# Optimization experiments

Hardware: AMD Instinct MI355X
Metric: run time of the kernel (lower is better)

Reference implementation:

```python
import jax, jax.numpy as jnp
import numpy as np

N_RES = 3      # n_resblock (weights SHARED across layers, matching [block]*n in torch)
N_E = 1024     # n_embeddings
E_DIM = 64     # dim_embeddings
P = 4
BETA = 0.25
B = 16384      # batch rows
IN = 128       # input_size
DENC = 512     # dim_encoder
DOUT = E_DIM * P  # dim_encoder_out = 256


def setup_inputs() -> dict:
    key = jax.random.key(0)
    ks = jax.random.split(key, 16)
    def w(k, o, i):
        return jax.random.normal(k, (o, i), jnp.float32) * 0.02
    return {
        "x": jax.random.normal(ks[0], (B, IN), jnp.float32),
        "a": jax.random.normal(ks[1], (B, IN), jnp.float32),
        "scale": 1.0 + 0.1 * jax.random.normal(ks[2], (IN,), jnp.float32),
        "shift": 0.01 * jax.random.normal(ks[3], (IN,), jnp.float32),
        "enc_win_w": w(ks[4], DENC, IN), "enc_win_b": jnp.zeros((DENC,), jnp.float32),
        "enc_ain_w": w(ks[5], DENC, IN), "enc_ain_b": jnp.zeros((DENC,), jnp.float32),
        "enc_wres_w": w(ks[6], DENC, DENC), "enc_wres_b": jnp.zeros((DENC,), jnp.float32),
        "enc_wres_g": jnp.ones((DENC,), jnp.float32), "enc_wres_be": jnp.zeros((DENC,), jnp.float32),
        "enc_ares_w": w(ks[7], DENC, DENC), "enc_ares_b": jnp.zeros((DENC,), jnp.float32),
        "enc_ares_g": jnp.ones((DENC,), jnp.float32), "enc_ares_be": jnp.zeros((DENC,), jnp.float32),
        "enc_out_w": w(ks[8], DOUT, DENC), "enc_out_b": jnp.zeros((DOUT,), jnp.float32),
        "dec1_w": w(ks[9], DENC, DOUT), "dec1_b": jnp.zeros((DENC,), jnp.float32),
        "dec_res_w": w(ks[10], DENC, DENC), "dec_res_b": jnp.zeros((DENC,), jnp.float32),
        "dec_res_g": jnp.ones((DENC,), jnp.float32), "dec_res_be": jnp.zeros((DENC,), jnp.float32),
        "dec2_w": w(ks[11], IN, DENC), "dec2_b": jnp.zeros((IN,), jnp.float32),
        "codebook": jax.random.uniform(ks[12], (N_E, E_DIM), jnp.float32, -1.0 / N_E, 1.0 / N_E),
    }


def _ln(h, g, b, eps=1e-5):
    m = jnp.mean(h, axis=-1, keepdims=True)
    v = jnp.var(h, axis=-1, keepdims=True)
    return (h - m) * jax.lax.rsqrt(v + eps) * g + b


def _resblock(x, w, b, g, be):
    # Linear -> LayerNorm -> ReLU, residual add
    h = x @ w.T + b
    return x + jax.nn.relu(_ln(h, g, be))


def reference(x, a, scale, shift,
              enc_win_w, enc_win_b, enc_ain_w, enc_ain_b,
              enc_wres_w, enc_wres_b, enc_wres_g, enc_wres_be,
              enc_ares_w, enc_ares_b, enc_ares_g, enc_ares_be,
              enc_out_w, enc_out_b,
              dec1_w, dec1_b,
              dec_res_w, dec_res_b, dec_res_g, dec_res_be,
              dec2_w, dec2_b, codebook):
    sg = jax.lax.stop_gradient
    # --- input normalization ---
    xs = (x - shift) / scale
    # --- Encoder (weight path modulated by activation-magnitude path) ---
    av = a @ enc_ain_w.T + enc_ain_b
    h = xs @ enc_win_w.T + enc_win_b
    for _ in range(N_RES):  # shared weights per stack, interleaved mul
        av = _resblock(av, enc_ares_w, enc_ares_b, enc_ares_g, enc_ares_be)
        h = _resblock(h, enc_wres_w, enc_wres_b, enc_wres_g, enc_wres_be) * av
    z_e = h @ enc_out_w.T + enc_out_b  # (B, P*E_DIM)
    # --- Vector quantization (cdist + argmin + gather) ---
    zf = z_e.reshape(-1, E_DIM)  # (B*P, E_DIM)
    d = (jnp.sum(zf * zf, axis=1, keepdims=True)
         + jnp.sum(codebook * codebook, axis=1)
         - 2.0 * zf @ codebook.T)  # (B*P, N_E)
    idx = jnp.argmin(d, axis=1)  # (B*P,)
    z_q = codebook[idx].reshape(z_e.shape)
    loss = (jnp.mean((sg(z_q) - z_e) ** 2)
            + BETA * jnp.mean((z_q - sg(z_e)) ** 2))
    z_q_st = z_e + sg(z_q - z_e)  # straight-through
    counts = jnp.zeros((N_E,), jnp.float32).at[idx].add(1.0)
    e_mean = counts / zf.shape[0]
    perplexity = jnp.exp(-jnp.sum(e_mean * jnp.log(e_mean + 1e-10)))
    # --- Decoder ---
    hd = z_q_st @ dec1_w.T + dec1_b
    for _ in range(N_RES):
        hd = _resblock(hd, dec_res_w, dec_res_b, dec_res_g, dec_res_be)
    x_hat = hd @ dec2_w.T + dec2_b
    x_hat = scale * x_hat + shift
    return (loss, x_hat, perplexity, z_q_st, idx)
```

## Files before the change

kernel.cpp:

```cpp
#include <hip/hip_runtime.h>
#include <hip/hip_bf16.h>
#include <math.h>

static constexpr int BROWS = 16384;
static constexpr int IND   = 128;
static constexpr int DE    = 512;
static constexpr int DOUTD = 256;
static constexpr int ED    = 64;
static constexpr int NE    = 1024;

static constexpr size_t O_XHAT = 1;
static constexpr size_t O_PERP = 2097153;
static constexpr size_t O_ZQ   = 2097154;
static constexpr size_t O_IDX  = 6291458;

typedef __attribute__((ext_vector_type(8))) short short8v;
typedef __attribute__((ext_vector_type(4))) float f32x4;
typedef __attribute__((ext_vector_type(4))) unsigned short ushort4v;
typedef __attribute__((ext_vector_type(8))) unsigned short ushort8v;

__device__ inline float wave_sum(float v) {
#pragma unroll
    for (int o = 32; o >= 1; o >>= 1) v += __shfl_xor(v, o, 64);
    return v;
}

__device__ inline unsigned short f2bf(float f) {
    unsigned u = __float_as_uint(f);
    return (unsigned short)((u + 0x7FFFu + ((u >> 16) & 1u)) >> 16);
}
__device__ inline float bf2f(unsigned short b) {
    return __uint_as_float(((unsigned)b) << 16);
}
struct Split3 { unsigned short b0, b1, b2; };
__device__ inline Split3 split3(float v) {
    Split3 s;
    s.b0 = f2bf(v);  float r  = v - bf2f(s.b0);
    s.b1 = f2bf(r);  float r2 = r - bf2f(s.b1);
    s.b2 = f2bf(r2);
    return s;
}

template<int K, int EPI>
__device__ inline void gemm8_body(const unsigned short* __restrict__ A0, const unsigned short* __restrict__ A1,
                                  const unsigned short* __restrict__ A2,
                                  const unsigned short* __restrict__ W0, const unsigned short* __restrict__ W1,
                                  const unsigned short* __restrict__ W2,
                                  const float* __restrict__ bias, float* __restrict__ Cf,
                                  unsigned short* __restrict__ S0, unsigned short* __restrict__ S1,
                                  unsigned short* __restrict__ S2, int N,
                                  short (*As)[128 * 40], short (*Ws)[128 * 40])
{
    const int t = threadIdx.x;
    const int bm = blockIdx.x << 7, bn = blockIdx.y << 7;
    const int lane = t & 63, wid = t >> 6;
    const int wm = (wid >> 1) << 6, wn = (wid & 1) << 6;
    const int lr = lane & 15, lg = lane >> 4;
    const unsigned short* Ap[3] = {A0, A1, A2};
    const unsigned short* Wp[3] = {W0, W1, W2};
    f32x4 acc[4][4] = {};
    for (int k0 = 0; k0 < K; k0 += 32) {
#pragma unroll
        for (int p = 0; p < 3; ++p) {
#pragma unroll
            for (int s = 0; s < 2; ++s) {
                int c = t + (s << 8);
                int row = c >> 2, kc = (c & 3) << 3;
                *(short8v*)&As[p][row * 40 + kc] =
                    *(const short8v*)(Ap[p] + (size_t)(bm + row) * K + k0 + kc);
                *(short8v*)&Ws[p][row * 40 + kc] =
                    *(const short8v*)(Wp[p] + (size_t)(bn + row) * K + k0 + kc);
            }
        }
        __syncthreads();
        short8v bfr[3][4];
#pragma unroll
        for (int p = 0; p < 3; ++p)
#pragma unroll
            for (int nj = 0; nj < 4; ++nj)
                bfr[p][nj] = *(const short8v*)&Ws[p][(wn + nj * 16 + lr) * 40 + lg * 8];
#pragma unroll
        for (int mi = 0; mi < 4; ++mi) {
            short8v a0 = *(const short8v*)&As[0][(wm + mi * 16 + lr) * 40 + lg * 8];
            short8v a1 = *(const short8v*)&As[1][(wm + mi * 16 + lr) * 40 + lg * 8];
            short8v a2 = *(const short8v*)&As[2][(wm + mi * 16 + lr) * 40 + lg * 8];
#pragma unroll
            for (int nj = 0; nj < 4; ++nj) {
                f32x4 c = acc[mi][nj];
                c = __builtin_amdgcn_mfma_f32_16x16x32_bf16(a2, bfr[1][nj], c, 0, 0, 0);
                c = __builtin_amdgcn_mfma_f32_16x16x32_bf16(a1, bfr[2][nj], c, 0, 0, 0);
                c = __builtin_amdgcn_mfma_f32_16x16x32_bf16(a1, bfr[1][nj], c, 0, 0, 0);
                c = __builtin_amdgcn_mfma_f32_16x16x32_bf16(a2, bfr[0][nj], c, 0, 0, 0);
                c = __builtin_amdgcn_mfma_f32_16x16x32_bf16(a0, bfr[2][nj], c, 0, 0, 0);
                c = __builtin_amdgcn_mfma_f32_16x16x32_bf16(a1, bfr[0][nj], c, 0, 0, 0);
                c = __builtin_amdgcn_mfma_f32_16x16x32_bf16(a0, bfr[1][nj], c, 0, 0, 0);
                c = __builtin_amdgcn_mfma_f32_16x16x32_bf16(a0, bfr[0][nj], c, 0, 0, 0);
                acc[mi][nj] = c;
            }
        }
        __syncthreads();
    }
#pragma unroll
    for (int mi = 0; mi < 4; ++mi)
#pragma unroll
        for (int nj = 0; nj < 4; ++nj)
#pragma unroll
            for (int r = 0; r < 4; ++r) {
                int m = bm + wm + mi * 16 + lg * 4 + r;
                int n = bn + wn + nj * 16 + lr;
                float v = acc[mi][nj][r] + bias[n];
                if (EPI == 0) {
                    Cf[(size_t)m * N + n] = v;
                } else {
                    Split3 sp = split3(v);
                    S0[(size_t)m * N + n] = sp.b0;
                    S1[(size_t)m * N + n] = sp.b1;
                    S2[(size_t)m * N + n] = sp.b2;
                }
            }
}

template<int K>
__global__ __launch_bounds__(256)
void gemm8_k(const unsigned short* __restrict__ A0, const unsigned short* __restrict__ A1,
             const unsigned short* __restrict__ A2,
             const unsigned short* __restrict__ W0, const unsigned short* __restrict__ W1,
             const unsigned short* __restrict__ W2,
             const float* __restrict__ bias, float* __restrict__ C, int N)
{
    __shared__ short As[3][128 * 40];
    __shared__ short Ws[3][128 * 40];
    gemm8_body<K, 0>(A0, A1, A2, W0, W1, W2, bias, C, nullptr, nullptr, nullptr, N, As, Ws);
}

struct G8 { const unsigned short *A0, *A1, *A2, *W0, *W1, *W2; const float* bias;
            float* Cf; unsigned short *S0, *S1, *S2; };

template<int K, int EPI>
__global__ __launch_bounds__(256)
void gemm8pair_k(G8 ga, G8 gb, int N)
{
    __shared__ short As[3][128 * 40];
    __shared__ short Ws[3][128 * 40];
    const G8& g = (blockIdx.z == 0) ? ga : gb;
    gemm8_body<K, EPI>(g.A0, g.A1, g.A2, g.W0, g.W1, g.W2, g.bias, g.Cf,
                       g.S0, g.S1, g.S2, N, As, Ws);
}

template<int K, int EPI>
__global__ __launch_bounds__(256)
void gemmbf_k(const short* __restrict__ A, const short* __restrict__ W,
              const float* __restrict__ bias, float* __restrict__ C, int N,
              unsigned short* __restrict__ Cb,
              const float* __restrict__ escale, const float* __restrict__ eshift)
{
    __shared__ short As[128 * 40];
    __shared__ short Ws[128 * 40];
    const int t = threadIdx.x;
    const int bm = blockIdx.x << 7, bn = blockIdx.y << 7;
    const int lane = t & 63, wid = t >> 6;
    const int wm = (wid >> 1) << 6, wn = (wid & 1) << 6;
    const int lr = lane & 15, lg = lane >> 4;
    f32x4 acc[4][4] = {};
    for (int k0 = 0; k0 < K; k0 += 32) {
#pragma unroll
        for (int s = 0; s < 2; ++s) {
            int c = t + (s << 8);
            int row = c >> 2, kc = (c & 3) << 3;
            *(short8v*)&As[row * 40 + kc] = *(const short8v*)(A + (size_t)(bm + row) * K + k0 + kc);
            *(short8v*)&Ws[row * 40 + kc] = *(const short8v*)(W + (size_t)(bn + row) * K + k0 + kc);
        }
        __syncthreads();
        short8v af[4], bf[4];
#pragma unroll
        for (int mi = 0; mi < 4; ++mi) af[mi] = *(const short8v*)&As[(wm + mi * 16 + lr) * 40 + lg * 8];
#pragma unroll
        for (int nj = 0; nj < 4; ++nj) bf[nj] = *(const short8v*)&Ws[(wn + nj * 16 + lr) * 40 + lg * 8];
#pragma unroll
        for (int mi = 0; mi < 4; ++mi)
#pragma unroll
            for (int nj = 0; nj < 4; ++nj)
                acc[mi][nj] = __builtin_amdgcn_mfma_f32_16x16x32_bf16(af[mi], bf[nj], acc[mi][nj], 0, 0, 0);
        __syncthreads();
    }
#pragma unroll
    for (int mi = 0; mi < 4; ++mi)
#pragma unroll
        for (int nj = 0; nj < 4; ++nj)
#pragma unroll
            for (int r = 0; r < 4; ++r) {
                int m = bm + wm + mi * 16 + lg * 4 + r;
                int n = bn + wn + nj * 16 + lr;
                float v = acc[mi][nj][r] + bias[n];
                if (EPI == 2) v = escale[n] * v + eshift[n];
                C[(size_t)m * N + n] = v;
                if (EPI == 1) Cb[(size_t)m * N + n] = f2bf(v);
            }
}

__global__ __launch_bounds__(256)
void prep2_k(const float* __restrict__ x, const float* __restrict__ scale,
             const float* __restrict__ shift,
             unsigned short* __restrict__ x0, unsigned short* __restrict__ x1,
             unsigned short* __restrict__ x2,
             const float* __restrict__ a,
             unsigned short* __restrict__ a0, unsigned short* __restrict__ a1,
             unsigned short* __restrict__ a2)
{
    if (blockIdx.x < 2048) {
        int g = blockIdx.x * 256 + threadIdx.x;
        float4 v = *(const float4*)(x + (size_t)g * 4);
        int col = (g * 4) & (IND - 1);
        float vals[4] = {v.x, v.y, v.z, v.w};
        ushort4v o0, o1, o2;
#pragma unroll
        for (int i = 0; i < 4; ++i) {
            float xs = (vals[i] - shift[col + i]) / scale[col + i];
            Split3 s = split3(xs);
            o0[i] = s.b0; o1[i] = s.b1; o2[i] = s.b2;
        }
        *(ushort4v*)(x0 + (size_t)g * 4) = o0;
        *(ushort4v*)(x1 + (size_t)g * 4) = o1;
        *(ushort4v*)(x2 + (size_t)g * 4) = o2;
    } else {
        int g = (blockIdx.x - 2048) * 256 + threadIdx.x;
        float4 v = *(const float4*)(a + (size_t)g * 4);
        float vals[4] = {v.x, v.y, v.z, v.w};
        ushort4v o0, o1, o2;
#pragma unroll
        for (int i = 0; i < 4; ++i) {
            Split3 s = split3(vals[i]);
            o0[i] = s.b0; o1[i] = s.b1; o2[i] = s.b2;
        }
        *(ushort4v*)(a0 + (size_t)g * 4) = o0;
        *(ushort4v*)(a1 + (size_t)g * 4) = o1;
        *(ushort4v*)(a2 + (size_t)g * 4) = o2;
    }
}

__global__ __launch_bounds__(256)
void wsplit_k(const float* __restrict__ ain_w, const float* __restrict__ win_w,
              const float* __restrict__ ares_w, const float* __restrict__ wres_w,
              const float* __restrict__ out_w,
              unsigned short* __restrict__ wsb)
{
    int g4 = blockIdx.x * 256 + threadIdx.x;
    const float* src; unsigned short *d0, *d1, *d2; int base;
    if (g4 < 16384)       { src = ain_w;  d0 = wsb;           d1 = wsb + 65536;   d2 = wsb + 131072;  base = 0; }
    else if (g4 < 32768)  { src = win_w;  d0 = wsb + 196608;  d1 = wsb + 262144;  d2 = wsb + 327680;  base = 16384; }
    else if (g4 < 98304)  { src = ares_w; d0 = wsb + 393216;  d1 = wsb + 655360;  d2 = wsb + 917504;  base = 32768; }
    else if (g4 < 163840) { src = wres_w; d0 = wsb + 1179648; d1 = wsb + 1441792; d2 = wsb + 1703936; base = 98304; }
    else                  { src = out_w;  d0 = wsb + 1966080; d1 = wsb + 2097152; d2 = wsb + 2228224; base = 163840; }
    int l4 = g4 - base;
    float4 v = *(const float4*)(src + (size_t)l4 * 4);
    float vals[4] = {v.x, v.y, v.z, v.w};
    ushort4v o0, o1, o2;
#pragma unroll
    for (int i = 0; i < 4; ++i) {
        Split3 s = split3(vals[i]);
        o0[i] = s.b0; o1[i] = s.b1; o2[i] = s.b2;
    }
    *(ushort4v*)(d0 + (size_t)l4 * 4) = o0;
    *(ushort4v*)(d1 + (size_t)l4 * 4) = o1;
    *(ushort4v*)(d2 + (size_t)l4 * 4) = o2;
}

__global__ __launch_bounds__(256)
void cvt3_k(const float* __restrict__ dec1_w, const float* __restrict__ dres_w,
            const float* __restrict__ dec2_w,
            unsigned short* __restrict__ w1b, unsigned short* __restrict__ wrb,
            unsigned short* __restrict__ w2b)
{
    int g = blockIdx.x * 256 + threadIdx.x;
    if (g < 131072)       w1b[g] = f2bf(dec1_w[g]);
    else if (g < 393216)  wrb[g - 131072] = f2bf(dres_w[g - 131072]);
    else if (g < 458752)  w2b[g - 393216] = f2bf(dec2_w[g - 393216]);
}

__global__ __launch_bounds__(256)
void ln_enc2s_k(const float* __restrict__ T1, const float* __restrict__ T2,
                unsigned short* __restrict__ a0, unsigned short* __restrict__ a1,
                unsigned short* __restrict__ a2,
                unsigned short* __restrict__ h0, unsigned short* __restrict__ h1,
                unsigned short* __restrict__ h2,
                const float* __restrict__ ag, const float* __restrict__ abe,
                const float* __restrict__ wg, const float* __restrict__ wbe)
{
    const int lane = threadIdx.x & 63;
    const int row  = (blockIdx.x << 2) + (threadIdx.x >> 6);
    const int col  = lane << 3;
    const size_t base = (size_t)row * DE + col;
    float t[8];
    { float4 p0 = *(const float4*)(T1 + base); float4 p1 = *(const float4*)(T1 + base + 4);
      t[0]=p0.x; t[1]=p0.y; t[2]=p0.z; t[3]=p0.w; t[4]=p1.x; t[5]=p1.y; t[6]=p1.z; t[7]=p1.w; }
    float s = 0.f;
#pragma unroll
    for (int i = 0; i < 8; ++i) s += t[i];
    s = wave_sum(s);
    float mean = s * (1.0f / 512.0f);
    float vs = 0.f;
#pragma unroll
    for (int i = 0; i < 8; ++i) { float d = t[i] - mean; vs += d * d; }
    vs = wave_sum(vs);
    float rstd = 1.0f / sqrtf(vs * (1.0f / 512.0f) + 1e-5f);
    float avn[8];
    {
        ushort8v b0 = *(const ushort8v*)(a0 + base);
        ushort8v b1 = *(const ushort8v*)(a1 + base);
        ushort8v b2 = *(const ushort8v*)(a2 + base);
        ushort8v o0, o1, o2;
#pragma unroll
        for (int i = 0; i < 8; ++i) {
            float avv = bf2f(b0[i]) + bf2f(b1[i]) + bf2f(b2[i]);
            float lnv = (t[i] - mean) * rstd * ag[col + i] + abe[col + i];
            avn[i] = avv + fmaxf(lnv, 0.0f);
            Split3 sp = split3(avn[i]);
            o0[i] = sp.b0; o1[i] = sp.b1; o2[i] = sp.b2;
        }
        *(ushort8v*)(a0 + base) = o0;
        *(ushort8v*)(a1 + base) = o1;
        *(ushort8v*)(a2 + base) = o2;
    }
    { float4 p0 = *(const float4*)(T2 + base); float4 p1 = *(const float4*)(T2 + base + 4);
      t[0]=p0.x; t[1]=p0.y; t[2]=p0.z; t[3]=p0.w; t[4]=p1.x; t[5]=p1.y; t[6]=p1.z; t[7]=p1.w; }
    s = 0.f;
#pragma unroll
    for (int i = 0; i < 8; ++i) s += t[i];
    s = wave_sum(s);
    float mean2 = s * (1.0f / 512.0f);
    vs = 0.f;
#pragma unroll
    for (int i = 0; i < 8; ++i) { float d = t[i] - mean2; vs += d * d; }
    vs = wave_sum(vs);
    float rstd2 = 1.0f / sqrtf(vs * (1.0f / 512.0f) + 1e-5f);
    {
        ushort8v b0 = *(const ushort8v*)(h0 + base);
        ushort8v b1 = *(const ushort8v*)(h1 + base);
        ushort8v b2 = *(const ushort8v*)(h2 + base);
        ushort8v o0, o1, o2;
#pragma unroll
        for (int i = 0; i < 8; ++i) {
            float hv  = bf2f(b0[i]) + bf2f(b1[i]) + bf2f(b2[i]);
            float lnv = (t[i] - mean2) * rstd2 * wg[col + i] + wbe[col + i];
            float hn  = (hv + fmaxf(lnv, 0.0f)) * avn[i];
            Split3 sp = split3(hn);
            o0[i] = sp.b0; o1[i] = sp.b1; o2[i] = sp.b2;
        }
        *(ushort8v*)(h0 + base) = o0;
        *(ushort8v*)(h1 + base) = o1;
        *(ushort8v*)(h2 + base) = o2;
    }
}

__global__ __launch_bounds__(256)
void ln_dec_k(const float* __restrict__ t_, float* __restrict__ h,
              const float* __restrict__ g, const float* __restrict__ be,
              unsigned short* __restrict__ hb)
{
    const int lane = threadIdx.x & 63;
    const int row  = (blockIdx.x << 2) + (threadIdx.x >> 6);
    const int col  = lane << 3;
    const size_t base = (size_t)row * DE + col;
    float t[8];
    { float4 p0 = *(const float4*)(t_ + base); float4 p1 = *(const float4*)(t_ + base + 4);
      t[0]=p0.x; t[1]=p0.y; t[2]=p0.z; t[3]=p0.w; t[4]=p1.x; t[5]=p1.y; t[6]=p1.z; t[7]=p1.w; }
    float s = 0.f;
#pragma unroll
    for (int i = 0; i < 8; ++i) s += t[i];
    s = wave_sum(s);
    float mean = s * (1.0f / 512.0f);
    float vs = 0.f;
#pragma unroll
    for (int i = 0; i < 8; ++i) { float d = t[i] - mean; vs += d * d; }
    vs = wave_sum(vs);
    float rstd = 1.0f / sqrtf(vs * (1.0f / 512.0f) + 1e-5f);
    float4 p0 = *(const float4*)(h + base); float4 p1 = *(const float4*)(h + base + 4);
    float hv[8] = {p0.x,p0.y,p0.z,p0.w,p1.x,p1.y,p1.z,p1.w};
    float hn[8];
    ushort8v ob;
#pragma unroll
    for (int i = 0; i < 8; ++i) {
        float lnv = (t[i] - mean) * rstd * g[col + i] + be[col + i];
        hn[i] = hv[i] + fmaxf(lnv, 0.0f);
        ob[i] = f2bf(hn[i]);
    }
    float4 o0 = {hn[0],hn[1],hn[2],hn[3]}, o1 = {hn[4],hn[5],hn[6],hn[7]};
    *(float4*)(h + base) = o0; *(float4*)(h + base + 4) = o1;
    *(ushort8v*)(hb + base) = ob;
}

__global__ __launch_bounds__(256)
void c2z_k(const float* __restrict__ cb, float* __restrict__ c2, int* __restrict__ counts,
           unsigned short* __restrict__ cbS0, unsigned short* __restrict__ cbS1,
           unsigned short* __restrict__ cbS2)
{
    int j = blockIdx.x * 256 + threadIdx.x;
    if (j < NE) {
        float s = 0.f;
        const float* p = cb + (size_t)j * ED;
#pragma unroll
        for (int d = 0; d < ED; ++d) s = fmaf(p[d], p[d], s);
        c2[j] = s;
        counts[j] = 0;
#pragma unroll
        for (int dc = 0; dc < 64; dc += 4) {
            float4 v = *(const float4*)(p + dc);
            float vals[4] = {v.x, v.y, v.z, v.w};
            ushort4v o0, o1, o2;
#pragma unroll
            for (int i = 0; i < 4; ++i) {
                Split3 sp = split3(vals[i]);
                o0[i] = sp.b0; o1[i] = sp.b1; o2[i] = sp.b2;
            }
            *(ushort4v*)(cbS0 + (size_t)j * 64 + dc) = o0;
            *(ushort4v*)(cbS1 + (size_t)j * 64 + dc) = o1;
            *(ushort4v*)(cbS2 + (size_t)j * 64 + dc) = o2;
        }
    }
}

__global__ __launch_bounds__(256)
void vq_k(const float* __restrict__ ze, const float* __restrict__ cb, const float* __restrict__ c2,
          const unsigned short* __restrict__ cbS0, const unsigned short* __restrict__ cbS1,
          const unsigned short* __restrict__ cbS2,
          float* __restrict__ idx_dst, float* __restrict__ zst_dst,
          unsigned short* __restrict__ zb,
          int* __restrict__ counts, float* __restrict__ partials)
{
    __shared__ unsigned short zA[3][64 * 64];
    __shared__ unsigned short cB[3][64 * 64];
    __shared__ float z2s[64];
    __shared__ float c2s[64];
    __shared__ int   bidxs[64];
    __shared__ float red[4];
    const int t = threadIdx.x;
    const int lane = t & 63, w = t >> 6;
    const size_t row0 = (size_t)blockIdx.x * 64;

#pragma unroll
    for (int s = 0; s < 2; ++s) {
        int c = t + (s << 8);
        int row = c >> 3, kb = c & 7;
        float4 v0 = *(const float4*)(ze + (row0 + row) * 64 + kb * 8);
        float4 v1 = *(const float4*)(ze + (row0 + row) * 64 + kb * 8 + 4);
        float vals[8] = {v0.x, v0.y, v0.z, v0.w, v1.x, v1.y, v1.z, v1.w};
        ushort8v o0, o1, o2;
#pragma unroll
        for (int i = 0; i < 8; ++i) {
            Split3 sp = split3(vals[i]);
            o0[i] = sp.b0; o1[i] = sp.b1; o2[i] = sp.b2;
        }
        int base = row * 64 + ((kb ^ (row & 7)) << 3);
        *(ushort8v*)&zA[0][base] = o0;
        *(ushort8v*)&zA[1][base] = o1;
        *(ushort8v*)&zA[2][base] = o2;
    }
    if (t < 64) {
        float z2 = 0.f;
        const float* zp = ze + (row0 + t) * 64;
#pragma unroll 8
        for (int d = 0; d < 64; ++d) z2 = fmaf(zp[d], zp[d], z2);
        z2s[t] = z2;
    }
    __syncthreads();

    short8v af[2][3];
    {
        int row = (w << 4) + (lane & 15);
#pragma unroll
        for (int ks = 0; ks < 2; ++ks) {
            int kb = (lane >> 4) + ks * 4;
            int base = row * 64 + ((kb ^ (row & 7)) << 3);
#pragma unroll
            for (int p = 0; p < 3; ++p)
                af[ks][p] = *(const short8v*)&zA[p][base];
        }
    }

    float best[4] = {INFINITY, INFINITY, INFINITY, INFINITY};
    int   bid[4]  = {0, 0, 0, 0};
    for (int t0 = 0; t0 < NE; t0 += 64) {
        __syncthreads();
#pragma unroll
        for (int s = 0; s < 2; ++s) {
            int c = t + (s << 8);
            int code = c >> 3, kb = c & 7;
            int gbase = (t0 + code) * 64 + kb * 8;
            int lbase = code * 64 + ((kb ^ (code & 7)) << 3);
            *(ushort8v*)&cB[0][lbase] = *(const ushort8v*)(cbS0 + gbase);
            *(ushort8v*)&cB[1][lbase] = *(const ushort8v*)(cbS1 + gbase);
            *(ushort8v*)&cB[2][lbase] = *(const ushort8v*)(cbS2 + gbase);
        }
        if (t < 64) c2s[t] = c2[t0 + t];
        __syncthreads();

#pragma unroll
        for (int ct = 0; ct < 4; ++ct) {
            f32x4 acc = {0.f, 0.f, 0.f, 0.f};
            int code = (ct << 4) + (lane & 15);
#pragma unroll
            for (int ks = 0; ks < 2; ++ks) {
                int kb = (lane >> 4) + ks * 4;
                int base = code * 64 + ((kb ^ (code & 7)) << 3);
                short8v b0 = *(const short8v*)&cB[0][base];
                short8v b1 = *(const short8v*)&cB[1][base];
                short8v b2 = *(const short8v*)&cB[2][base];
                acc = __builtin_amdgcn_mfma_f32_16x16x32_bf16(af[ks][2], b1, acc, 0, 0, 0);
                acc = __builtin_amdgcn_mfma_f32_16x16x32_bf16(af[ks][1], b2, acc, 0, 0, 0);
                acc = __builtin_amdgcn_mfma_f32_16x16x32_bf16(af[ks][1], b1, acc, 0, 0, 0);
                acc = __builtin_amdgcn_mfma_f32_16x16x32_bf16(af[ks][2], b0, acc, 0, 0, 0);
                acc = __builtin_amdgcn_mfma_f32_16x16x32_bf16(af[ks][0], b2, acc, 0, 0, 0);
                acc = __builtin_amdgcn_mfma_f32_16x16x32_bf16(af[ks][1], b0, acc, 0, 0, 0);
                acc = __builtin_amdgcn_mfma_f32_16x16x32_bf16(af[ks][0], b1, acc, 0, 0, 0);
                acc = __builtin_amdgcn_mfma_f32_16x16x32_bf16(af[ks][0], b0, acc, 0, 0, 0);
            }
            float c2v = c2s[(ct << 4) + (lane & 15)];
            int gcode = t0 + (ct << 4) + (lane & 15);
#pragma unroll
            for (int r = 0; r < 4; ++r) {
                float z2v = z2s[(w << 4) + ((lane >> 4) << 2) + r];
                float term = __fadd_rn(z2v, c2v);
                float dist = __fsub_rn(term, __fmul_rn(2.0f, acc[r]));
                if (dist < best[r]) { best[r] = dist; bid[r] = gcode; }
            }
        }
    }
#pragma unroll
    for (int r = 0; r < 4; ++r) {
        float bd = best[r]; int bi = bid[r];
#pragma unroll
        for (int m = 1; m < 16; m <<= 1) {
            float od = __shfl_xor(bd, m, 64);
            int   oi = __shfl_xor(bi, m, 64);
            if (od < bd || (od == bd && oi < bi)) { bd = od; bi = oi; }
        }
        if ((lane & 15) == 0) {
            int row = (w << 4) + ((lane >> 4) << 2) + r;
            bidxs[row] = bi;
            idx_dst[row0 + row] = (float)bi;
            atomicAdd(&counts[bi], 1);
        }
    }
    __syncthreads();
    const int row = t >> 2, cq = t & 3;
    const int bi = bidxs[row];
    float lsum = 0.f;
#pragma unroll
    for (int dd = 0; dd < 16; dd += 4) {
        int d0 = (cq << 4) + dd;
        float4 q4 = *(const float4*)(cb + (size_t)bi * 64 + d0);
        float qv[4] = {q4.x, q4.y, q4.z, q4.w};
        float4 zv4 = *(const float4*)(ze + (row0 + row) * 64 + d0);
        float zvv[4] = {zv4.x, zv4.y, zv4.z, zv4.w};
        float zst[4];
#pragma unroll
        for (int i = 0; i < 4; ++i) {
            float zv = zvv[i];
            float df = qv[i] - zv;
            lsum = fmaf(df, df, lsum);
            zst[i] = __fadd_rn(zv, __fsub_rn(qv[i], zv));
            zb[(row0 + row) * 64 + d0 + i] = f2bf(zst[i]);
        }
        float2 o0 = {zst[0], zst[1]}, o1 = {zst[2], zst[3]};
        *(float2*)(zst_dst + (row0 + row) * 64 + d0) = o0;
        *(float2*)(zst_dst + (row0 + row) * 64 + d0 + 2) = o1;
    }
    lsum = wave_sum(lsum);
    if ((t & 63) == 0) red[t >> 6] = lsum;
    __syncthreads();
    if (t == 0) partials[blockIdx.x] = ((red[0] + red[1]) + red[2]) + red[3];
}

__global__ __launch_bounds__(256)
void fin_k(const float* __restrict__ partials, const int* __restrict__ counts,
           float* __restrict__ loss_out, float* __restrict__ perp_out)
{
    __shared__ float red[4];
    __shared__ float red2[4];
    const int tid = threadIdx.x;
    float v = 0.f;
    for (int c = tid; c < 1024; c += 256) v += partials[c];
    float s = wave_sum(v);
    if ((tid & 63) == 0) red[tid >> 6] = s;
    float ep = 0.f;
    for (int c = tid; c < NE; c += 256) {
        float e = (float)counts[c] * (1.0f / 65536.0f);
        ep += e * logf(e + 1e-10f);
    }
    ep = wave_sum(ep);
    if ((tid & 63) == 0) red2[tid >> 6] = ep;
    __syncthreads();
    if (tid == 0) {
        float S = ((red[0] + red[1]) + red[2]) + red[3];
        float E = ((red2[0] + red2[1]) + red2[2]) + red2[3];
        loss_out[0] = 1.25f * (S * (1.0f / 4194304.0f));
        perp_out[0] = expf(-E);
    }
}

extern "C" void kernel_launch(void* const* d_in, const int* in_sizes, int n_in,
                              void* d_out, int out_size, void* d_ws, size_t ws_size,
                              hipStream_t stream)
{
    const float* x       = (const float*)d_in[0];
    const float* a       = (const float*)d_in[1];
    const float* scale   = (const float*)d_in[2];
    const float* shift   = (const float*)d_in[3];
    const float* win_w   = (const float*)d_in[4];
    const float* win_b   = (const float*)d_in[5];
    const float* ain_w   = (const float*)d_in[6];
    const float* ain_b   = (const float*)d_in[7];
    const float* wres_w  = (const float*)d_in[8];
    const float* wres_b  = (const float*)d_in[9];
    const float* wres_g  = (const float*)d_in[10];
    const float* wres_be = (const float*)d_in[11];
    const float* ares_w  = (const float*)d_in[12];
    const float* ares_b  = (const float*)d_in[13];
    const float* ares_g  = (const float*)d_in[14];
    const float* ares_be = (const float*)d_in[15];
    const float* out_w   = (const float*)d_in[16];
    const float* out_b   = (const float*)d_in[17];
    const float* dec1_w  = (const float*)d_in[18];
    const float* dec1_b  = (const float*)d_in[19];
    const float* dres_w  = (const float*)d_in[20];
    const float* dres_b  = (const float*)d_in[21];
    const float* dres_g  = (const float*)d_in[22];
    const float* dres_be = (const float*)d_in[23];
    const float* dec2_w  = (const float*)d_in[24];
    const float* dec2_b  = (const float*)d_in[25];
    const float* cb      = (const float*)d_in[26];

    float* ws = (float*)d_ws;
    unsigned short* u = (unsigned short*)d_ws;
    unsigned short* avS0 = u;
    unsigned short* avS1 = u + 8388608;
    unsigned short* avS2 = u + 16777216;
    unsigned short* hS0  = u + 25165824;
    unsigned short* hS1  = u + 33554432;
    unsigned short* hS2  = u + 41943040;
    float* T1 = ws + 25165824;
    float* T2 = ws + 29360128;
    float* ZE = ws + 25165824;
    unsigned short* aS0  = u + 50331648, *aS1  = u + 52428800, *aS2  = u + 54525952;
    unsigned short* xsS0 = u + 56623104, *xsS1 = u + 58720256, *xsS2 = u + 60817408;
    unsigned short* ZB  = u;
    unsigned short* w1b = u + 4194304;
    unsigned short* wrb = u + 4325376;
    unsigned short* w2b = u + 4587520;
    float* t_dec = ws + 4194304;
    float* hd    = ws + 12582912;
    unsigned short* Hb = (unsigned short*)(ws + 29360128);
    unsigned short* wsb = u + 67108864;
    unsigned short* ainS0 = wsb,            *ainS1 = wsb + 65536,  *ainS2 = wsb + 131072;
    unsigned short* winS0 = wsb + 196608,   *winS1 = wsb + 262144, *winS2 = wsb + 327680;
    unsigned short* areS0 = wsb + 393216,   *areS1 = wsb + 655360, *areS2 = wsb + 917504;
    unsigned short* wreS0 = wsb + 1179648,  *wreS1 = wsb + 1441792,*wreS2 = wsb + 1703936;
    unsigned short* outS0 = wsb + 1966080,  *outS1 = wsb + 2097152,*outS2 = wsb + 2228224;
    float* c2v      = ws + 34800000;
    int*   counts   = (int*)(ws + 34801024);
    float* partials = ws + 34802048;
    unsigned short* cbS0 = u + 69606144;
    unsigned short* cbS1 = u + 69671680;
    unsigned short* cbS2 = u + 69737216;

    float* dout = (float*)d_out;

    wsplit_k<<<768, 256, 0, stream>>>(ain_w, win_w, ares_w, wres_w, out_w, wsb);
    prep2_k<<<4096, 256, 0, stream>>>(x, scale, shift, xsS0, xsS1, xsS2, a, aS0, aS1, aS2);
    {
        G8 ga = {aS0, aS1, aS2, ainS0, ainS1, ainS2, ain_b, nullptr, avS0, avS1, avS2};
        G8 gb = {xsS0, xsS1, xsS2, winS0, winS1, winS2, win_b, nullptr, hS0, hS1, hS2};
        gemm8pair_k<128, 1><<<dim3(128, 4, 2), 256, 0, stream>>>(ga, gb, DE);
    }
    for (int r = 0; r < 3; ++r) {
        for (int half = 0; half < 2; ++half) {
            const size_t mo = (size_t)half * 8192 * DE;
            G8 ga = {avS0 + mo, avS1 + mo, avS2 + mo, areS0, areS1, areS2, ares_b, T1, nullptr, nullptr, nullptr};
            G8 gb = {hS0 + mo,  hS1 + mo,  hS2 + mo,  wreS0, wreS1, wreS2, wres_b, T2, nullptr, nullptr, nullptr};
            gemm8pair_k<512, 0><<<dim3(64, 4, 2), 256, 0, stream>>>(ga, gb, DE);
            ln_enc2s_k<<<2048, 256, 0, stream>>>(T1, T2,
                avS0 + mo, avS1 + mo, avS2 + mo, hS0 + mo, hS1 + mo, hS2 + mo,
                ares_g, ares_be, wres_g, wres_be);
        }
    }
    gemm8_k<512><<<dim3(128, 2), 256, 0, stream>>>(hS0, hS1, hS2, outS0, outS1, outS2, out_b, ZE, DOUTD);
    c2z_k<<<4, 256, 0, stream>>>(cb, c2v, counts, cbS0, cbS1, cbS2);
    vq_k<<<1024, 256, 0, stream>>>(ZE, cb, c2v, cbS0, cbS1, cbS2,
                                   dout + O_IDX, dout + O_ZQ, ZB, counts, partials);
    fin_k<<<1, 256, 0, stream>>>(partials, counts, dout, dout + O_PERP);
    cvt3_k<<<1792, 256, 0, stream>>>(dec1_w, dres_w, dec2_w, w1b, wrb, w2b);
    gemmbf_k<256, 1><<<dim3(128, 4), 256, 0, stream>>>(
        (const short*)ZB, (const short*)w1b, dec1_b, hd, DE, Hb, nullptr, nullptr);
    for (int r = 0; r < 3; ++r) {
        gemmbf_k<512, 0><<<dim3(128, 4), 256, 0, stream>>>(
            (const short*)Hb, (const short*)wrb, dres_b, t_dec, DE, nullptr, nullptr, nullptr);
        ln_dec_k<<<4096, 256, 0, stream>>>(t_dec, hd, dres_g, dres_be, Hb);
    }
    gemmbf_k<512, 2><<<dim3(128, 1), 256, 0, stream>>>(
        (const short*)Hb, (const short*)w2b, dec2_b, dout + O_XHAT, IND, nullptr, scale, shift);
}
```

Measured before the change: 817.2 us.

## Merge prep kernels and double-buffer codebook tiles in VQ kernel

Folds the weight split, input split and codebook norm/split kernels into one launch, which removes two kernel launches and their gaps. In the VQ kernel, codebook tiles are now double-buffered in shared memory: the next tile is loaded into registers while MFMAs run on the current one, and only one barrier is taken per tile instead of two. The c2 values are read straight from global memory rather than staged in shared memory. The cvt3 launch is moved earlier in the stream; this does not change the total work.

Result: faster. 789.8 us (-3.4%).

```diff
diff --git a/kernel.cpp b/kernel.cpp
--- a/kernel.cpp
+++ b/kernel.cpp
@@ -199,32 +199,32 @@
 }
 
 __global__ __launch_bounds__(256)
-void prep2_k(const float* __restrict__ x, const float* __restrict__ scale,
-             const float* __restrict__ shift,
-             unsigned short* __restrict__ x0, unsigned short* __restrict__ x1,
-             unsigned short* __restrict__ x2,
-             const float* __restrict__ a,
-             unsigned short* __restrict__ a0, unsigned short* __restrict__ a1,
-             unsigned short* __restrict__ a2)
-{
-    if (blockIdx.x < 2048) {
-        int g = blockIdx.x * 256 + threadIdx.x;
-        float4 v = *(const float4*)(x + (size_t)g * 4);
-        int col = (g * 4) & (IND - 1);
-        float vals[4] = {v.x, v.y, v.z, v.w};
-        ushort4v o0, o1, o2;
-#pragma unroll
-        for (int i = 0; i < 4; ++i) {
-            float xs = (vals[i] - shift[col + i]) / scale[col + i];
-            Split3 s = split3(xs);
-            o0[i] = s.b0; o1[i] = s.b1; o2[i] = s.b2;
-        }
-        *(ushort4v*)(x0 + (size_t)g * 4) = o0;
-        *(ushort4v*)(x1 + (size_t)g * 4) = o1;
-        *(ushort4v*)(x2 + (size_t)g * 4) = o2;
-    } else {
-        int g = (blockIdx.x - 2048) * 256 + threadIdx.x;
-        float4 v = *(const float4*)(a + (size_t)g * 4);
+void pre_k(const float* __restrict__ x, const float* __restrict__ scale,
+           const float* __restrict__ shift,
+           unsigned short* __restrict__ x0, unsigned short* __restrict__ x1,
+           unsigned short* __restrict__ x2,
+           const float* __restrict__ a,
+           unsigned short* __restrict__ a0, unsigned short* __restrict__ a1,
+           unsigned short* __restrict__ a2,
+           const float* __restrict__ ain_w, const float* __restrict__ win_w,
+           const float* __restrict__ ares_w, const float* __restrict__ wres_w,
+           const float* __restrict__ out_w, unsigned short* __restrict__ wsb,
+           const float* __restrict__ cb, float* __restrict__ c2, int* __restrict__ counts,
+           unsigned short* __restrict__ cbS0, unsigned short* __restrict__ cbS1,
+           unsigned short* __restrict__ cbS2)
+{
+    const int b = blockIdx.x;
+    const int t = threadIdx.x;
+    if (b < 768) {
+        int g4 = b * 256 + t;
+        const float* src; unsigned short *d0, *d1, *d2; int base;
+        if (g4 < 16384)       { src = ain_w;  d0 = wsb;           d1 = wsb + 65536;   d2 = wsb + 131072;  base = 0; }
+        else if (g4 < 32768)  { src = win_w;  d0 = wsb + 196608;  d1 = wsb + 262144;  d2 = wsb + 327680;  base = 16384; }
+        else if (g4 < 98304)  { src = ares_w; d0 = wsb + 393216;  d1 = wsb + 655360;  d2 = wsb + 917504;  base = 32768; }
+        else if (g4 < 163840) { src = wres_w; d0 = wsb + 1179648; d1 = wsb + 1441792; d2 = wsb + 1703936; base = 98304; }
+        else                  { src = out_w;  d0 = wsb + 1966080; d1 = wsb + 2097152; d2 = wsb + 2228224; base = 163840; }
+        int l4 = g4 - base;
+        float4 v = *(const float4*)(src + (size_t)l4 * 4);
         float vals[4] = {v.x, v.y, v.z, v.w};
         ushort4v o0, o1, o2;
 #pragma unroll
@@ -232,37 +232,65 @@
             Split3 s = split3(vals[i]);
             o0[i] = s.b0; o1[i] = s.b1; o2[i] = s.b2;
         }
-        *(ushort4v*)(a0 + (size_t)g * 4) = o0;
-        *(ushort4v*)(a1 + (size_t)g * 4) = o1;
-        *(ushort4v*)(a2 + (size_t)g * 4) = o2;
-    }
-}
-
-__global__ __launch_bounds__(256)
-void wsplit_k(const float* __restrict__ ain_w, const float* __restrict__ win_w,
-              const float* __restrict__ ares_w, const float* __restrict__ wres_w,
-              const float* __restrict__ out_w,
-              unsigned short* __restrict__ wsb)
-{
-    int g4 = blockIdx.x * 256 + threadIdx.x;
-    const float* src; unsigned short *d0, *d1, *d2; int base;
-    if (g4 < 16384)       { src = ain_w;  d0 = wsb;           d1 = wsb + 65536;   d2 = wsb + 131072;  base = 0; }
-    else if (g4 < 32768)  { src = win_w;  d0 = wsb + 196608;  d1 = wsb + 262144;  d2 = wsb + 327680;  base = 16384; }
-    else if (g4 < 98304)  { src = ares_w; d0 = wsb + 393216;  d1 = wsb + 655360;  d2 = wsb + 917504;  base = 32768; }
-    else if (g4 < 163840) { src = wres_w; d0 = wsb + 1179648; d1 = wsb + 1441792; d2 = wsb + 1703936; base = 98304; }
-    else                  { src = out_w;  d0 = wsb + 1966080; d1 = wsb + 2097152; d2 = wsb + 2228224; base = 163840; }
-    int l4 = g4 - base;
-    float4 v = *(const float4*)(src + (size_t)l4 * 4);
-    float vals[4] = {v.x, v.y, v.z, v.w};
-    ushort4v o0, o1, o2;
-#pragma unroll
-    for (int i = 0; i < 4; ++i) {
-        Split3 s = split3(vals[i]);
-        o0[i] = s.b0; o1[i] = s.b1; o2[i] = s.b2;
-    }
-    *(ushort4v*)(d0 + (size_t)l4 * 4) = o0;
-    *(ushort4v*)(d1 + (size_t)l4 * 4) = o1;
-    *(ushort4v*)(d2 + (size_t)l4 * 4) = o2;
+        *(ushort4v*)(d0 + (size_t)l4 * 4) = o0;
+        *(ushort4v*)(d1 + (size_t)l4 * 4) = o1;
+        *(ushort4v*)(d2 + (size_t)l4 * 4) = o2;
+    } else if (b < 4864) {
+        int bb = b - 768;
+        if (bb < 2048) {
+            int g = bb * 256 + t;
+            float4 v = *(const float4*)(x + (size_t)g * 4);
+            int col = (g * 4) & (IND - 1);
+            float vals[4] = {v.x, v.y, v.z, v.w};
+            ushort4v o0, o1, o2;
+#pragma unroll
+            for (int i = 0; i < 4; ++i) {
+                float xs = (vals[i] - shift[col + i]) / scale[col + i];
+                Split3 s = split3(xs);
+                o0[i] = s.b0; o1[i] = s.b1; o2[i] = s.b2;
+            }
+            *(ushort4v*)(x0 + (size_t)g * 4) = o0;
+            *(ushort4v*)(x1 + (size_t)g * 4) = o1;
+            *(ushort4v*)(x2 + (size_t)g * 4) = o2;
+        } else {
+            int g = (bb - 2048) * 256 + t;
+            float4 v = *(const float4*)(a + (size_t)g * 4);
+            float vals[4] = {v.x, v.y, v.z, v.w};
+            ushort4v o0, o1, o2;
+#pragma unroll
+            for (int i = 0; i < 4; ++i) {
+                Split3 s = split3(vals[i]);
+                o0[i] = s.b0; o1[i] = s.b1; o2[i] = s.b2;
+            }
+            *(ushort4v*)(a0 + (size_t)g * 4) = o0;
+            *(ushort4v*)(a1 + (size_t)g * 4) = o1;
+            *(ushort4v*)(a2 + (size_t)g * 4) = o2;
+        }
+    } else {
+        int j = (b - 4864) * 256 + t;
+        if (j < NE) {
+            float s = 0.f;
+            const float* p = cb + (size_t)j * ED;
+#pragma unroll
+            for (int d = 0; d < ED; ++d) s = fmaf(p[d], p[d], s);
+            c2[j] = s;
+            counts[j] = 0;
+#pragma unroll
+            for (int dc = 0; dc < 64; dc += 4) {
+                float4 v = *(const float4*)(p + dc);
+                float vals[4] = {v.x, v.y, v.z, v.w};
+                ushort4v o0, o1, o2;
+#pragma unroll
+                for (int i = 0; i < 4; ++i) {
+                    Split3 sp = split3(vals[i]);
+                    o0[i] = sp.b0; o1[i] = sp.b1; o2[i] = sp.b2;
+                }
+                *(ushort4v*)(cbS0 + (size_t)j * 64 + dc) = o0;
+                *(ushort4v*)(cbS1 + (size_t)j * 64 + dc) = o1;
+                *(ushort4v*)(cbS2 + (size_t)j * 64 + dc) = o2;
+            }
+        }
+    }
 }
 
 __global__ __launch_bounds__(256)
@@ -390,36 +418,6 @@
 }
 
 __global__ __launch_bounds__(256)
-void c2z_k(const float* __restrict__ cb, float* __restrict__ c2, int* __restrict__ counts,
-           unsigned short* __restrict__ cbS0, unsigned short* __restrict__ cbS1,
-           unsigned short* __restrict__ cbS2)
-{
-    int j = blockIdx.x * 256 + threadIdx.x;
-    if (j < NE) {
-        float s = 0.f;
-        const float* p = cb + (size_t)j * ED;
-#pragma unroll
-        for (int d = 0; d < ED; ++d) s = fmaf(p[d], p[d], s);
-        c2[j] = s;
-        counts[j] = 0;
-#pragma unroll
-        for (int dc = 0; dc < 64; dc += 4) {
-            float4 v = *(const float4*)(p + dc);
-            float vals[4] = {v.x, v.y, v.z, v.w};
-            ushort4v o0, o1, o2;
-#pragma unroll
-            for (int i = 0; i < 4; ++i) {
-                Split3 sp = split3(vals[i]);
-                o0[i] = sp.b0; o1[i] = sp.b1; o2[i] = sp.b2;
-            }
-            *(ushort4v*)(cbS0 + (size_t)j * 64 + dc) = o0;
-            *(ushort4v*)(cbS1 + (size_t)j * 64 + dc) = o1;
-            *(ushort4v*)(cbS2 + (size_t)j * 64 + dc) = o2;
-        }
-    }
-}
-
-__global__ __launch_bounds__(256)
 void vq_k(const float* __restrict__ ze, const float* __restrict__ cb, const float* __restrict__ c2,
           const unsigned short* __restrict__ cbS0, const unsigned short* __restrict__ cbS1,
           const unsigned short* __restrict__ cbS2,
@@ -427,10 +425,8 @@
           unsigned short* __restrict__ zb,
           int* __restrict__ counts, float* __restrict__ partials)
 {
-    __shared__ unsigned short zA[3][64 * 64];
-    __shared__ unsigned short cB[3][64 * 64];
+    __shared__ unsigned short P[2][3][64 * 64];
     __shared__ float z2s[64];
-    __shared__ float c2s[64];
     __shared__ int   bidxs[64];
     __shared__ float red[4];
     const int t = threadIdx.x;
@@ -451,9 +447,13 @@
             o0[i] = sp.b0; o1[i] = sp.b1; o2[i] = sp.b2;
         }
         int base = row * 64 + ((kb ^ (row & 7)) << 3);
-        *(ushort8v*)&zA[0][base] = o0;
-        *(ushort8v*)&zA[1][base] = o1;
-        *(ushort8v*)&zA[2][base] = o2;
+        *(ushort8v*)&P[1][0][base] = o0;
+        *(ushort8v*)&P[1][1][base] = o1;
+        *(ushort8v*)&P[1][2][base] = o2;
+        int gbase = row * 64 + kb * 8;
+        *(ushort8v*)&P[0][0][base] = *(const ushort8v*)(cbS0 + gbase);
+        *(ushort8v*)&P[0][1][base] = *(const ushort8v*)(cbS1 + gbase);
+        *(ushort8v*)&P[0][2][base] = *(const ushort8v*)(cbS2 + gbase);
     }
     if (t < 64) {
         float z2 = 0.f;
@@ -473,27 +473,28 @@
             int base = row * 64 + ((kb ^ (row & 7)) << 3);
 #pragma unroll
             for (int p = 0; p < 3; ++p)
-                af[ks][p] = *(const short8v*)&zA[p][base];
-        }
-    }
+                af[ks][p] = *(const short8v*)&P[1][p][base];
+        }
+    }
+    __syncthreads();
 
     float best[4] = {INFINITY, INFINITY, INFINITY, INFINITY};
     int   bid[4]  = {0, 0, 0, 0};
-    for (int t0 = 0; t0 < NE; t0 += 64) {
-        __syncthreads();
-#pragma unroll
-        for (int s = 0; s < 2; ++s) {
-            int c = t + (s << 8);
-            int code = c >> 3, kb = c & 7;
-            int gbase = (t0 + code) * 64 + kb * 8;
-            int lbase = code * 64 + ((kb ^ (code & 7)) << 3);
-            *(ushort8v*)&cB[0][lbase] = *(const ushort8v*)(cbS0 + gbase);
-            *(ushort8v*)&cB[1][lbase] = *(const ushort8v*)(cbS1 + gbase);
-            *(ushort8v*)&cB[2][lbase] = *(const ushort8v*)(cbS2 + gbase);
-        }
-        if (t < 64) c2s[t] = c2[t0 + t];
-        __syncthreads();
-
+    for (int tt = 0; tt < 16; ++tt) {
+        const int cur = tt & 1;
+        ushort8v nx0[2], nx1[2], nx2[2];
+        if (tt < 15) {
+#pragma unroll
+            for (int s = 0; s < 2; ++s) {
+                int c = t + (s << 8);
+                int code = c >> 3, kb = c & 7;
+                size_t gbase = (size_t)((tt + 1) * 64 + code) * 64 + kb * 8;
+                nx0[s] = *(const ushort8v*)(cbS0 + gbase);
+                nx1[s] = *(const ushort8v*)(cbS1 + gbase);
+                nx2[s] = *(const ushort8v*)(cbS2 + gbase);
+            }
+        }
+        const int t0 = tt << 6;
 #pragma unroll
         for (int ct = 0; ct < 4; ++ct) {
             f32x4 acc = {0.f, 0.f, 0.f, 0.f};
@@ -502,9 +503,9 @@
             for (int ks = 0; ks < 2; ++ks) {
                 int kb = (lane >> 4) + ks * 4;
                 int base = code * 64 + ((kb ^ (code & 7)) << 3);
-                short8v b0 = *(const short8v*)&cB[0][base];
-                short8v b1 = *(const short8v*)&cB[1][base];
-                short8v b2 = *(const short8v*)&cB[2][base];
+                short8v b0 = *(const short8v*)&P[cur][0][base];
+                short8v b1 = *(const short8v*)&P[cur][1][base];
+                short8v b2 = *(const short8v*)&P[cur][2][base];
                 acc = __builtin_amdgcn_mfma_f32_16x16x32_bf16(af[ks][2], b1, acc, 0, 0, 0);
                 acc = __builtin_amdgcn_mfma_f32_16x16x32_bf16(af[ks][1], b2, acc, 0, 0, 0);
                 acc = __builtin_amdgcn_mfma_f32_16x16x32_bf16(af[ks][1], b1, acc, 0, 0, 0);
@@ -514,8 +515,8 @@
                 acc = __builtin_amdgcn_mfma_f32_16x16x32_bf16(af[ks][0], b1, acc, 0, 0, 0);
                 acc = __builtin_amdgcn_mfma_f32_16x16x32_bf16(af[ks][0], b0, acc, 0, 0, 0);
             }
-            float c2v = c2s[(ct << 4) + (lane & 15)];
-            int gcode = t0 + (ct << 4) + (lane & 15);
+            float c2v = c2[t0 + code];
+            int gcode = t0 + code;
 #pragma unroll
             for (int r = 0; r < 4; ++r) {
                 float z2v = z2s[(w << 4) + ((lane >> 4) << 2) + r];
@@ -524,6 +525,18 @@
                 if (dist < best[r]) { best[r] = dist; bid[r] = gcode; }
             }
         }
+        if (tt < 15) {
+#pragma unroll
+            for (int s = 0; s < 2; ++s) {
+                int c = t + (s << 8);
+                int code = c >> 3, kb = c & 7;
+                int base = code * 64 + ((kb ^ (code & 7)) << 3);
+                *(ushort8v*)&P[cur ^ 1][0][base] = nx0[s];
+                *(ushort8v*)&P[cur ^ 1][1][base] = nx1[s];
+                *(ushort8v*)&P[cur ^ 1][2][base] = nx2[s];
+            }
+        }
+        __syncthreads();
     }
 #pragma unroll
     for (int r = 0; r < 4; ++r) {
@@ -665,8 +678,10 @@
 
     float* dout = (float*)d_out;
 
-    wsplit_k<<<768, 256, 0, stream>>>(ain_w, win_w, ares_w, wres_w, out_w, wsb);
-    prep2_k<<<4096, 256, 0, stream>>>(x, scale, shift, xsS0, xsS1, xsS2, a, aS0, aS1, aS2);
+    pre_k<<<4868, 256, 0, stream>>>(x, scale, shift, xsS0, xsS1, xsS2,
+                                    a, aS0, aS1, aS2,
+                                    ain_w, win_w, ares_w, wres_w, out_w, wsb,
+                                    cb, c2v, counts, cbS0, cbS1, cbS2);
     {
         G8 ga = {aS0, aS1, aS2, ainS0, ainS1, ainS2, ain_b, nullptr, avS0, avS1, avS2};
         G8 gb = {xsS0, xsS1, xsS2, winS0, winS1, winS2, win_b, nullptr, hS0, hS1, hS2};
@@ -684,11 +699,10 @@
         }
     }
     gemm8_k<512><<<dim3(128, 2), 256, 0, stream>>>(hS0, hS1, hS2, outS0, outS1, outS2, out_b, ZE, DOUTD);
-    c2z_k<<<4, 256, 0, stream>>>(cb, c2v, counts, cbS0, cbS1, cbS2);
+    cvt3_k<<<1792, 256, 0, stream>>>(dec1_w, dres_w, dec2_w, w1b, wrb, w2b);
     vq_k<<<1024, 256, 0, stream>>>(ZE, cb, c2v, cbS0, cbS1, cbS2,
                                    dout + O_IDX, dout + O_ZQ, ZB, counts, partials);
     fin_k<<<1, 256, 0, stream>>>(partials, counts, dout, dout + O_PERP);
-    cvt3_k<<<1792, 256, 0, stream>>>(dec1_w, dres_w, dec2_w, w1b, wrb, w2b);
     gemmbf_k<256, 1><<<dim3(128, 4), 256, 0, stream>>>(
         (const short*)ZB, (const short*)w1b, dec1_b, hd, DE, Hb, nullptr, nullptr);
     for (int r = 0; r < 3; ++r) {
```
